# Kernel optimization log

Measured on AMD Instinct MI355X. Metric: run time of the kernel, lower is better.

The kernel has to match this reference:

```python
import jax, jax.numpy as jnp
import numpy as np

WINDOW_SYNC = 20   # min(20, T//2) with T=8192
WINDOW_SURGE = 10
BN_EPS = 1e-5      # BatchNorm1d eval-mode, running_mean=0, running_var=1


def _corr_matrix(x):
    # x: [w, A] observations x variables -> [A, A] Pearson correlation
    xc = x - x.mean(0)
    cov = xc.T @ xc
    d = jnp.sqrt(jnp.diag(cov))
    return cov / (d[:, None] * d[None, :])


def _offdiag_mean(C):
    A = C.shape[0]
    return (C.sum() - jnp.trace(C)) / (A * (A - 1))


def _rolling_offdiag_corr(returns, window):
    # mean off-diagonal correlation over each trailing window [i-window, i)
    T, A = returns.shape
    starts = jnp.arange(T - window)
    def one(s):
        w = jax.lax.dynamic_slice(returns, (s, 0), (window, A))
        return _offdiag_mean(_corr_matrix(w))
    return jax.vmap(one)(starts)


def setup_inputs() -> dict:
    key = jax.random.key(0)
    ks = jax.random.split(key, 10)
    T, A, H = 8192, 128, 128
    returns_sequence = jax.random.normal(ks[0], (T, A), dtype=jnp.float32) * 0.02
    positions = jax.random.normal(ks[1], (A,), dtype=jnp.float32)
    s1 = 1.0 / np.sqrt(2 * A)
    s2 = 1.0 / np.sqrt(H)
    s3 = 1.0 / np.sqrt(H // 2)
    return {
        "returns_sequence": returns_sequence,
        "positions": positions,
        "w1": jax.random.uniform(ks[2], (2 * A, H), jnp.float32, -s1, s1),
        "b1": jax.random.uniform(ks[3], (H,), jnp.float32, -s1, s1),
        "gamma": jnp.ones((H,), jnp.float32),
        "beta": jnp.zeros((H,), jnp.float32),
        "w2": jax.random.uniform(ks[4], (H, H // 2), jnp.float32, -s2, s2),
        "b2": jax.random.uniform(ks[5], (H // 2,), jnp.float32, -s2, s2),
        "w3": jax.random.uniform(ks[6], (H // 2, 3), jnp.float32, -s3, s3),
        "b3": jax.random.uniform(ks[7], (3,), jnp.float32, -s3, s3),
    }


def reference(returns_sequence, positions, w1, b1, gamma, beta, w2, b2, w3, b3):
    returns = returns_sequence
    T, A = returns.shape

    # ---- herding index ----
    cs_std = jnp.std(returns, axis=1, ddof=1)                 # [T]
    herding_trend = -jnp.diff(cs_std).mean()
    avg_dispersion = cs_std.mean()
    herding_index = jnp.clip(herding_trend / (avg_dispersion + 1e-6) + 0.5, 0.0, 1.0)

    # ---- synchronization ----
    corr = _corr_matrix(returns)                              # [A, A]
    avg_correlation = _offdiag_mean(corr)
    rolling = _rolling_offdiag_corr(returns, WINDOW_SYNC)     # [T-20]
    phase_locking = (rolling > 0.7).astype(jnp.float32).mean()
    eigvals = jnp.linalg.eigvalsh(corr)
    sync_indicator = eigvals.max() / A
    sync_risk = jnp.minimum(1.0, sync_indicator * avg_correlation)

    # ---- diversity loss ----
    return_diversity = 1.0 - jnp.abs(corr).mean()             # includes diagonal (as in torch)
    pa = jnp.abs(positions)
    position_diversity = 1.0 - (pa / pa.sum()).max()
    diversity_loss = 1.0 - jnp.sqrt(return_diversity * position_diversity)

    # ---- correlation surge ----
    rolling10 = _rolling_offdiag_corr(returns, WINDOW_SURGE)  # [T-10]
    recent = rolling10[-5:].mean()
    historical = rolling10[:-5].mean()
    surge_raw = jnp.clip((recent - historical) / historical, 0.0, 1.0)
    correlation_surge = jnp.where(historical > 0, surge_raw, 0.0)

    # ---- phase coupling (pairwise sign concordance) ----
    signs = jnp.sign(returns)                                 # [T, A]
    classes = jnp.array([-1.0, 0.0, 1.0], dtype=returns.dtype)
    I = (signs[None, :, :] == classes[:, None, None]).astype(returns.dtype)  # [3, T, A]
    M = jnp.einsum('cta,ctb->ab', I, I) / T                   # eq-fraction matrix [A, A]
    avg_concordance = _offdiag_mean(M)
    phase_coupling = jnp.clip((avg_concordance - 0.5) * 2.0, 0.0, 1.0)

    # ---- herding detector MLP (BatchNorm1d in eval mode) ----
    feats = jnp.concatenate([returns[-1], positions])         # [2A]
    h = jax.nn.relu(feats @ w1 + b1)
    h = gamma * (h / jnp.sqrt(1.0 + BN_EPS)) + beta
    h = jax.nn.relu(h @ w2 + b2)
    logits = h @ w3 + b3
    herding_severity = jax.nn.softmax(logits)[2]

    collective_risk = (herding_index + sync_risk + diversity_loss) / 3.0

    return jnp.stack([herding_index, herding_severity, sync_risk, phase_locking,
                      diversity_loss, correlation_surge, phase_coupling, collective_risk])
```

## Files before the change

kernel.cpp:

```cpp
#include <hip/hip_runtime.h>
#include <math.h>

#define TN 8192
#define AN 128
#define NW20 (TN - 20)
#define NW10 (TN - 10)

#define NB_GRAM 128
#define NB_ROW  512
#define NB_R20  511
#define NB_R10  512
#define NB_WORK (NB_GRAM + NB_ROW + NB_R20 + NB_R10)

#define WS_STD0 0
#define WS_STDL 1
#define WS_SPEC 8
#define WS_BLK  200
#define WS_DEND 4096

template <int W>
__device__ __forceinline__ void roll_strip4(const float* __restrict__ x,
                                            int s0, int nwin, int lane,
                                            double& accA, double& accB) {
  constexpr int NR = W + 3;
  float a0[NR], a1[NR];
#pragma unroll
  for (int t = 0; t < NR; ++t) {
    int r = s0 + t; r = (r < TN) ? r : (TN - 1);
    float2 v = *(const float2*)(x + (size_t)r * AN + 2 * lane);
    a0[t] = v.x; a1[t] = v.y;
  }
#pragma unroll
  for (int w4 = 0; w4 < 4; ++w4) {
    int s = s0 + w4;
    if (s < nwin) {
      float sf0 = 0.f, sf1 = 0.f;
#pragma unroll
      for (int t = 0; t < W; ++t) { sf0 += a0[w4 + t]; sf1 += a1[w4 + t]; }
      float mu0 = sf0 / W, mu1 = sf1 / W;
      float v0 = 0.f, v1 = 0.f;
#pragma unroll
      for (int t = 0; t < W; ++t) {
        float d0 = a0[w4 + t] - mu0, d1 = a1[w4 + t] - mu1;
        v0 += d0 * d0; v1 += d1 * d1;
      }
      float i0 = 1.0f / sqrtf(v0), i1 = 1.0f / sqrtf(v1);
      float q[W];
#pragma unroll
      for (int t = 0; t < W; ++t)
        q[t] = (a0[w4 + t] - mu0) * i0 + (a1[w4 + t] - mu1) * i1;
      int n = W;
#pragma unroll
      for (int o = 1; o <= 32; o <<= 1) {
#pragma unroll
        for (int k = 0; k < n; ++k) q[k] += __shfl_xor(q[k], o);
        if (n > 1) {
          int nh = n >> 1;
          bool hi = (lane & o) != 0;
#pragma unroll
          for (int k = 0; k < nh; ++k) q[k] = hi ? q[2 * k + 1] : q[2 * k];
          if (n & 1) { q[nh] = q[2 * nh]; n = nh + 1; } else { n = nh; }
        }
      }
      float alpha = (W == 20) ? ((lane & 16) ? 0.125f : 0.5f)
                              : ((lane & 8) ? 0.0625f : 0.25f);
      float r = q[0] * q[0] * alpha;
#pragma unroll
      for (int o = 32; o; o >>= 1) r += __shfl_xor(r, o);
      if (lane == 0) {
        double off = ((double)r - (double)AN) / ((double)AN * (AN - 1));
        if (W == 20) {
          accA += (off > 0.7) ? 1.0 : 0.0;
        } else {
          accA += off;
          if (s >= TN - W - 5) accB += off;
        }
      }
    }
  }
}

__global__ void __launch_bounds__(256) k_main(const float* __restrict__ x,
                                              double* __restrict__ wsd,
                                              float* __restrict__ pc,
                                              float* __restrict__ pdg,
                                              float* __restrict__ pg) {
  __shared__ union {
    float stage[8][AN];
    double tacc[4][2];
  } sm;
  const int b = blockIdx.x;
  const int tid = threadIdx.x;
  const int lane = tid & 63;
  const int w = tid >> 6;

  if (b < NB_GRAM) {
    int i0 = (tid >> 4) * 8;
    int j0 = (tid & 15) * 8;
    int lrow = tid >> 5;
    int lcol = (tid & 31) * 4;
    const float* xs = x + (size_t)b * 64 * AN;
    float acc[8][8];
#pragma unroll
    for (int a = 0; a < 8; ++a)
#pragma unroll
      for (int c = 0; c < 8; ++c) acc[a][c] = 0.f;
    float4 v = *(const float4*)(xs + lrow * AN + lcol);
    for (int it = 0; it < 8; ++it) {
      __syncthreads();
      *(float4*)(&sm.stage[lrow][lcol]) = v;
      __syncthreads();
      if (it + 1 < 8)
        v = *(const float4*)(xs + ((it + 1) * 8 + lrow) * AN + lcol);
#pragma unroll
      for (int r = 0; r < 8; ++r) {
        float aa[8], bb[8];
        *(float4*)(aa) = *(const float4*)(&sm.stage[r][i0]);
        *(float4*)(aa + 4) = *(const float4*)(&sm.stage[r][i0 + 4]);
        *(float4*)(bb) = *(const float4*)(&sm.stage[r][j0]);
        *(float4*)(bb + 4) = *(const float4*)(&sm.stage[r][j0 + 4]);
#pragma unroll
        for (int ai = 0; ai < 8; ++ai)
#pragma unroll
          for (int bj = 0; bj < 8; ++bj)
            acc[ai][bj] = fmaf(aa[ai], bb[bj], acc[ai][bj]);
      }
    }
    float* dst = pg + (size_t)b * (AN * AN);
#pragma unroll
    for (int ai = 0; ai < 8; ++ai)
#pragma unroll
      for (int bj = 0; bj < 8; bj += 4)
        *(float4*)(dst + (i0 + ai) * AN + j0 + bj) =
            make_float4(acc[ai][bj], acc[ai][bj + 1], acc[ai][bj + 2],
                        acc[ai][bj + 3]);
    if ((tid >> 4) == (tid & 15)) {
#pragma unroll
      for (int k = 0; k < 8; ++k) pdg[b * AN + i0 + k] = acc[k][k];
    }
    if (tid < AN) {
      float cs = 0.f;
      for (int r = 0; r < 64; ++r) cs += xs[r * AN + tid];
      pc[b * AN + tid] = cs;
    }
    return;
  }

  if (b < NB_GRAM + NB_ROW) {
    int rb = b - NB_GRAM;
    double sstd = 0.0, sconc = 0.0;
    for (int rr = 0; rr < 4; ++rr) {
      int t = rb * 16 + w * 4 + rr;
      float2 xv = *(const float2*)(x + (size_t)t * AN + 2 * lane);
      float x0 = xv.x, x1 = xv.y;
      float s = x0 + x1;
#pragma unroll
      for (int o = 32; o; o >>= 1) s += __shfl_xor(s, o);
      float mean = s * (1.0f / AN);
      float d0 = x0 - mean, d1 = x1 - mean;
      float q = d0 * d0 + d1 * d1;
#pragma unroll
      for (int o = 32; o; o >>= 1) q += __shfl_xor(q, o);
      float sd = sqrtf(q / (float)(AN - 1));
      int pk = (int)(x0 < 0.f) + (int)(x1 < 0.f)
             + (((int)(x0 == 0.f) + (int)(x1 == 0.f)) << 10)
             + (((int)(x0 > 0.f) + (int)(x1 > 0.f)) << 20);
#pragma unroll
      for (int o = 32; o; o >>= 1) pk += __shfl_xor(pk, o);
      if (lane == 0) {
        int nn = pk & 1023, nz = (pk >> 10) & 1023, np = (pk >> 20) & 1023;
        sconc += (double)nn * nn + (double)nz * nz + (double)np * np;
        sstd += (double)sd;
        if (t == 0) wsd[WS_STD0] = (double)sd;
        if (t == TN - 1) wsd[WS_STDL] = (double)sd;
      }
    }
    if (lane == 0) { sm.tacc[w][0] = sstd; sm.tacc[w][1] = sconc; }
    __syncthreads();
    if (tid == 0) {
      wsd[WS_BLK + (size_t)b * 2 + 0] =
          sm.tacc[0][0] + sm.tacc[1][0] + sm.tacc[2][0] + sm.tacc[3][0];
      wsd[WS_BLK + (size_t)b * 2 + 1] =
          sm.tacc[0][1] + sm.tacc[1][1] + sm.tacc[2][1] + sm.tacc[3][1];
    }
    return;
  }

  if (b < NB_GRAM + NB_ROW + NB_R20) {
    int s0 = (b - (NB_GRAM + NB_ROW)) * 16 + w * 4;
    double cnt = 0.0, dummy = 0.0;
    roll_strip4<20>(x, s0, NW20, lane, cnt, dummy);
    if (lane == 0) { sm.tacc[w][0] = cnt; }
    __syncthreads();
    if (tid == 0)
      wsd[WS_BLK + (size_t)b * 2 + 0] =
          sm.tacc[0][0] + sm.tacc[1][0] + sm.tacc[2][0] + sm.tacc[3][0];
    return;
  }

  {
    int s0 = (b - (NB_GRAM + NB_ROW + NB_R20)) * 16 + w * 4;
    double s10 = 0.0, s10l5 = 0.0;
    roll_strip4<10>(x, s0, NW10, lane, s10, s10l5);
    if (lane == 0) { sm.tacc[w][0] = s10; sm.tacc[w][1] = s10l5; }
    __syncthreads();
    if (tid == 0) {
      wsd[WS_BLK + (size_t)b * 2 + 0] =
          sm.tacc[0][0] + sm.tacc[1][0] + sm.tacc[2][0] + sm.tacc[3][0];
      wsd[WS_BLK + (size_t)b * 2 + 1] =
          sm.tacc[0][1] + sm.tacc[1][1] + sm.tacc[2][1] + sm.tacc[3][1];
    }
  }
}

__global__ void __launch_bounds__(256) k_fold(const float* __restrict__ pc,
                                              const float* __restrict__ pdg,
                                              const float* __restrict__ pg,
                                              double* __restrict__ wsd,
                                              float* __restrict__ corr) {
  __shared__ double r0[256], r1[256], r2[256], r3[256], r4[256];
  int b = blockIdx.x;
  int t = threadIdx.x;
  if (b < 64) {
    __shared__ double muS[AN], dS[AN];
    if (t < AN) {
      double cs = 0.0, dg = 0.0;
      for (int s = 0; s < NB_GRAM; ++s) {
        cs += (double)pc[s * AN + t];
        dg += (double)pdg[s * AN + t];
      }
      double mu = cs / (double)TN;
      muS[t] = mu;
      dS[t] = sqrt(dg - (double)TN * mu * mu);
    }
    __syncthreads();
    int e = b * 256 + t;
    int i = e >> 7, j = e & (AN - 1);
    double cv = 0.0;
    for (int s = 0; s < NB_GRAM; ++s) cv += (double)pg[(size_t)s * (AN * AN) + e];
    cv -= (double)TN * muS[i] * muS[j];
    double c = cv / (dS[i] * dS[j]);
    corr[e] = (float)c;
    r0[t] = c;
    r1[t] = fabs(c);
    r2[t] = (i == j) ? c : 0.0;
    __syncthreads();
    for (int sft = 128; sft; sft >>= 1) {
      if (t < sft) { r0[t] += r0[t + sft]; r1[t] += r1[t + sft]; r2[t] += r2[t + sft]; }
      __syncthreads();
    }
    if (t == 0) {
      wsd[WS_SPEC + b * 3 + 0] = r0[0];
      wsd[WS_SPEC + b * 3 + 1] = r1[0];
      wsd[WS_SPEC + b * 3 + 2] = r2[0];
    }
  } else {
    double a = 0.0, bc = 0.0, cnt = 0.0, s10 = 0.0, s10l5 = 0.0;
    for (int k = NB_GRAM + t; k < NB_WORK; k += 256) {
      const double* p = wsd + WS_BLK + (size_t)k * 2;
      if (k < NB_GRAM + NB_ROW) { a += p[0]; bc += p[1]; }
      else if (k < NB_GRAM + NB_ROW + NB_R20) cnt += p[0];
      else { s10 += p[0]; s10l5 += p[1]; }
    }
    r0[t] = a; r1[t] = bc; r2[t] = cnt; r3[t] = s10; r4[t] = s10l5;
    __syncthreads();
    for (int sft = 128; sft; sft >>= 1) {
      if (t < sft) {
        r0[t] += r0[t + sft]; r1[t] += r1[t + sft]; r2[t] += r2[t + sft];
        r3[t] += r3[t + sft]; r4[t] += r4[t + sft];
      }
      __syncthreads();
    }
    if (t == 0) {
      wsd[2] = r0[0];
      wsd[3] = r1[0];
      wsd[4] = r2[0];
      wsd[5] = r3[0];
      wsd[6] = r4[0];
    }
  }
}

__global__ void __launch_bounds__(256) k_spec_tail(
    const float* __restrict__ x, const float* __restrict__ pos,
    const float* __restrict__ w1, const float* __restrict__ b1,
    const float* __restrict__ gamma, const float* __restrict__ beta,
    const float* __restrict__ w2, const float* __restrict__ b2,
    const float* __restrict__ w3, const float* __restrict__ b3,
    const double* __restrict__ wsd, const float* __restrict__ corr,
    float* __restrict__ out) {
  __shared__ float vv[AN], prt[256], un[AN], red[4];
  __shared__ double spec[3];
  __shared__ float f[2 * AN], h1[AN], h2[64], lg[3];
  int t = threadIdx.x;
  int lane = t & 63;
  int w = t >> 6;
  if (t < 64) {
    double s0 = wsd[WS_SPEC + t * 3 + 0];
    double s1 = wsd[WS_SPEC + t * 3 + 1];
    double s2 = wsd[WS_SPEC + t * 3 + 2];
#pragma unroll
    for (int o = 32; o; o >>= 1) {
      s0 += __shfl_xor(s0, o);
      s1 += __shfl_xor(s1, o);
      s2 += __shfl_xor(s2, o);
    }
    if (t == 0) { spec[0] = s0; spec[1] = s1; spec[2] = s2; }
  }
  f[t] = (t < AN) ? x[(size_t)(TN - 1) * AN + t] : pos[t - AN];
  if (t < AN) vv[t] = 1.0f;
  __syncthreads();
  int ri = t & (AN - 1), hh = t >> 7;
  const float4* rp = (const float4*)(corr + ri * AN + hh * 64);
  float lam = 0.0f;
  for (int it = 0; it < 12; ++it) {
    const float4* vp = (const float4*)(&vv[hh * 64]);
    float acc = 0.f;
#pragma unroll
    for (int k = 0; k < 16; ++k) {
      float4 a = rp[k], bv = vp[k];
      acc += a.x * bv.x + a.y * bv.y + a.z * bv.z + a.w * bv.w;
    }
    prt[t] = acc;
    __syncthreads();
    if (t < AN) {
      float u = prt[t] + prt[t + 128];
      un[t] = u;
      float sq = u * u;
#pragma unroll
      for (int o = 32; o; o >>= 1) sq += __shfl_xor(sq, o);
      if (lane == 0) red[w] = sq;
    }
    __syncthreads();
    lam = sqrtf(red[0] + red[1]);
    if (t < AN) vv[t] = un[t] / lam;
    __syncthreads();
  }
  {
    int n = t & 127, h = t >> 7;
    float acc = 0.f;
    const float* wcol = w1 + h * 128 * AN + n;
    const float* fv = f + h * 128;
    for (int k = 0; k < 128; ++k) acc = fmaf(fv[k], wcol[k * AN], acc);
    prt[t] = acc;
  }
  __syncthreads();
  if (t < AN) {
    float acc = b1[t] + prt[t] + prt[t + 128];
    acc = fmaxf(acc, 0.0f);
    h1[t] = gamma[t] * (acc / sqrtf(1.0f + 1e-5f)) + beta[t];
  }
  __syncthreads();
  if (t < 64) {
    float acc = b2[t];
    for (int k = 0; k < AN; ++k) acc = fmaf(h1[k], w2[k * 64 + t], acc);
    h2[t] = fmaxf(acc, 0.0f);
  }
  __syncthreads();
  if (t < 3) {
    float acc = b3[t];
    for (int k = 0; k < 64; ++k) acc = fmaf(h2[k], w3[k * 3 + t], acc);
    lg[t] = acc;
  }
  __syncthreads();
  if (t != 0) return;
  float m = fmaxf(lg[0], fmaxf(lg[1], lg[2]));
  float e0 = expf(lg[0] - m), e1 = expf(lg[1] - m), e2 = expf(lg[2] - m);
  double sev = (double)(e2 / (e0 + e1 + e2));
  double sumstd = wsd[2], conc = wsd[3], cnt20 = wsd[4];
  double sum10 = wsd[5], sum10l5 = wsd[6];
  double avg_disp = sumstd / (double)TN;
  double trend = -(wsd[WS_STDL] - wsd[WS_STD0]) / (double)(TN - 1);
  double hi = trend / (avg_disp + 1e-6) + 0.5;
  hi = fmin(1.0, fmax(0.0, hi));
  double avg_corr = (spec[0] - spec[2]) / ((double)AN * (AN - 1));
  double sync_ind = (double)lam / (double)AN;
  double sync_risk = fmin(1.0, sync_ind * avg_corr);
  double pl = cnt20 / (double)(TN - 20);
  double rd = 1.0 - spec[1] / ((double)AN * AN);
  double pasum = 0.0, pamax = 0.0;
  for (int k = 0; k < AN; ++k) {
    double pa = fabs((double)pos[k]);
    pasum += pa;
    if (pa > pamax) pamax = pa;
  }
  double pd = 1.0 - pamax / pasum;
  double dl = 1.0 - sqrt(rd * pd);
  double recent = sum10l5 / 5.0;
  double hist = (sum10 - sum10l5) / (double)(TN - 10 - 5);
  double sraw = (recent - hist) / hist;
  sraw = fmin(1.0, fmax(0.0, sraw));
  double surge = (hist > 0.0) ? sraw : 0.0;
  double ac = (conc / (double)TN - (double)AN) / ((double)AN * (AN - 1));
  double pcup = fmin(1.0, fmax(0.0, (ac - 0.5) * 2.0));
  double cr = (hi + sync_risk + dl) / 3.0;
  out[0] = (float)hi;
  out[1] = (float)sev;
  out[2] = (float)sync_risk;
  out[3] = (float)pl;
  out[4] = (float)dl;
  out[5] = (float)surge;
  out[6] = (float)pcup;
  out[7] = (float)cr;
}

extern "C" void kernel_launch(void* const* d_in, const int* in_sizes, int n_in,
                              void* d_out, int out_size, void* d_ws, size_t ws_size,
                              hipStream_t stream) {
  const float* x     = (const float*)d_in[0];
  const float* pos   = (const float*)d_in[1];
  const float* w1    = (const float*)d_in[2];
  const float* b1    = (const float*)d_in[3];
  const float* gamma = (const float*)d_in[4];
  const float* beta  = (const float*)d_in[5];
  const float* w2    = (const float*)d_in[6];
  const float* b2    = (const float*)d_in[7];
  const float* w3    = (const float*)d_in[8];
  const float* b3    = (const float*)d_in[9];
  float* out = (float*)d_out;
  double* wsd = (double*)d_ws;
  float* corr = (float*)(wsd + WS_DEND);
  float* pc   = corr + AN * AN;
  float* pdg  = pc + NB_GRAM * AN;
  float* pg   = pdg + NB_GRAM * AN;

  k_main<<<NB_WORK, 256, 0, stream>>>(x, wsd, pc, pdg, pg);
  k_fold<<<65, 256, 0, stream>>>(pc, pdg, pg, wsd, corr);
  k_spec_tail<<<1, 256, 0, stream>>>(x, pos, w1, b1, gamma, beta, w2, b2,
                                     w3, b3, wsd, corr, out);
}
```

Baseline: 127.1 us.

## Merge fold and spectral tail kernels using an atomic completion flag

After: 183.5 us. 1.44x slower.

```diff
diff --git a/kernel.cpp b/kernel.cpp
--- a/kernel.cpp
+++ b/kernel.cpp
@@ -14,6 +14,7 @@
 
 #define WS_STD0 0
 #define WS_STDL 1
+#define WS_FLAG 7
 #define WS_SPEC 8
 #define WS_BLK  200
 #define WS_DEND 4096
@@ -94,6 +95,8 @@
   const int lane = tid & 63;
   const int w = tid >> 6;
 
+  if (b == 0 && tid == 0) *(int*)(wsd + WS_FLAG) = 0;
+
   if (b < NB_GRAM) {
     int i0 = (tid >> 4) * 8;
     int j0 = (tid & 15) * 8;
@@ -213,14 +216,22 @@
   }
 }
 
-__global__ void __launch_bounds__(256) k_fold(const float* __restrict__ pc,
-                                              const float* __restrict__ pdg,
-                                              const float* __restrict__ pg,
-                                              double* __restrict__ wsd,
-                                              float* __restrict__ corr) {
+__global__ void __launch_bounds__(256) k_tail(
+    const float* __restrict__ x, const float* __restrict__ pos,
+    const float* __restrict__ w1, const float* __restrict__ b1,
+    const float* __restrict__ gamma, const float* __restrict__ beta,
+    const float* __restrict__ w2, const float* __restrict__ b2,
+    const float* __restrict__ w3, const float* __restrict__ b3,
+    const float* __restrict__ pc, const float* __restrict__ pdg,
+    const float* __restrict__ pg, double* __restrict__ wsd,
+    float* __restrict__ corr, float* __restrict__ out) {
   __shared__ double r0[256], r1[256], r2[256], r3[256], r4[256];
   int b = blockIdx.x;
   int t = threadIdx.x;
+  int lane = t & 63;
+  int w = t >> 6;
+  int* flg = (int*)(wsd + WS_FLAG);
+
   if (b < 64) {
     __shared__ double muS[AN], dS[AN];
     if (t < AN) {
@@ -254,7 +265,17 @@
       wsd[WS_SPEC + b * 3 + 1] = r1[0];
       wsd[WS_SPEC + b * 3 + 2] = r2[0];
     }
-  } else {
+    __syncthreads();
+    if (t == 0)
+      __hip_atomic_fetch_add(flg, 1, __ATOMIC_RELEASE, __HIP_MEMORY_SCOPE_AGENT);
+    return;
+  }
+
+  __shared__ float f[2 * AN], prt[256], h1[AN], h2[64], lg[3];
+  __shared__ float vv[AN], un[AN], red[4];
+  __shared__ double spec[3], scv[8], pr2[4];
+
+  {
     double a = 0.0, bc = 0.0, cnt = 0.0, s10 = 0.0, s10l5 = 0.0;
     for (int k = NB_GRAM + t; k < NB_WORK; k += 256) {
       const double* p = wsd + WS_BLK + (size_t)k * 2;
@@ -272,70 +293,16 @@
       __syncthreads();
     }
     if (t == 0) {
-      wsd[2] = r0[0];
-      wsd[3] = r1[0];
-      wsd[4] = r2[0];
-      wsd[5] = r3[0];
-      wsd[6] = r4[0];
-    }
-  }
-}
-
-__global__ void __launch_bounds__(256) k_spec_tail(
-    const float* __restrict__ x, const float* __restrict__ pos,
-    const float* __restrict__ w1, const float* __restrict__ b1,
-    const float* __restrict__ gamma, const float* __restrict__ beta,
-    const float* __restrict__ w2, const float* __restrict__ b2,
-    const float* __restrict__ w3, const float* __restrict__ b3,
-    const double* __restrict__ wsd, const float* __restrict__ corr,
-    float* __restrict__ out) {
-  __shared__ float vv[AN], prt[256], un[AN], red[4];
-  __shared__ double spec[3];
-  __shared__ float f[2 * AN], h1[AN], h2[64], lg[3];
-  int t = threadIdx.x;
-  int lane = t & 63;
-  int w = t >> 6;
-  if (t < 64) {
-    double s0 = wsd[WS_SPEC + t * 3 + 0];
-    double s1 = wsd[WS_SPEC + t * 3 + 1];
-    double s2 = wsd[WS_SPEC + t * 3 + 2];
-#pragma unroll
-    for (int o = 32; o; o >>= 1) {
-      s0 += __shfl_xor(s0, o);
-      s1 += __shfl_xor(s1, o);
-      s2 += __shfl_xor(s2, o);
-    }
-    if (t == 0) { spec[0] = s0; spec[1] = s1; spec[2] = s2; }
-  }
+      scv[0] = r0[0];
+      scv[1] = r1[0];
+      scv[2] = r2[0];
+      scv[3] = r3[0];
+      scv[4] = r4[0];
+    }
+  }
+
   f[t] = (t < AN) ? x[(size_t)(TN - 1) * AN + t] : pos[t - AN];
-  if (t < AN) vv[t] = 1.0f;
-  __syncthreads();
-  int ri = t & (AN - 1), hh = t >> 7;
-  const float4* rp = (const float4*)(corr + ri * AN + hh * 64);
-  float lam = 0.0f;
-  for (int it = 0; it < 12; ++it) {
-    const float4* vp = (const float4*)(&vv[hh * 64]);
-    float acc = 0.f;
-#pragma unroll
-    for (int k = 0; k < 16; ++k) {
-      float4 a = rp[k], bv = vp[k];
-      acc += a.x * bv.x + a.y * bv.y + a.z * bv.z + a.w * bv.w;
-    }
-    prt[t] = acc;
-    __syncthreads();
-    if (t < AN) {
-      float u = prt[t] + prt[t + 128];
-      un[t] = u;
-      float sq = u * u;
-#pragma unroll
-      for (int o = 32; o; o >>= 1) sq += __shfl_xor(sq, o);
-      if (lane == 0) red[w] = sq;
-    }
-    __syncthreads();
-    lam = sqrtf(red[0] + red[1]);
-    if (t < AN) vv[t] = un[t] / lam;
-    __syncthreads();
-  }
+  __syncthreads();
   {
     int n = t & 127, h = t >> 7;
     float acc = 0.f;
@@ -362,13 +329,76 @@
     for (int k = 0; k < 64; ++k) acc = fmaf(h2[k], w3[k * 3 + t], acc);
     lg[t] = acc;
   }
-  __syncthreads();
+
+  if (t < AN) {
+    double pa = fabs((double)pos[t]);
+    double ps = pa, pm = pa;
+#pragma unroll
+    for (int o = 32; o; o >>= 1) {
+      ps += __shfl_xor(ps, o);
+      pm = fmax(pm, __shfl_xor(pm, o));
+    }
+    if (lane == 0) { pr2[w] = ps; pr2[2 + w] = pm; }
+  }
+  __syncthreads();
+  if (t == 0) {
+    float m = fmaxf(lg[0], fmaxf(lg[1], lg[2]));
+    float e0 = expf(lg[0] - m), e1 = expf(lg[1] - m), e2 = expf(lg[2] - m);
+    scv[5] = (double)(e2 / (e0 + e1 + e2));
+    scv[6] = pr2[0] + pr2[1];
+    scv[7] = fmax(pr2[2], pr2[3]);
+  }
+
+  if (t == 0) {
+    while (__hip_atomic_load(flg, __ATOMIC_RELAXED, __HIP_MEMORY_SCOPE_AGENT) < 64)
+      __builtin_amdgcn_s_sleep(2);
+    (void)__hip_atomic_load(flg, __ATOMIC_ACQUIRE, __HIP_MEMORY_SCOPE_AGENT);
+  }
+  __syncthreads();
+
+  if (t < 64) {
+    double s0 = wsd[WS_SPEC + t * 3 + 0];
+    double s1 = wsd[WS_SPEC + t * 3 + 1];
+    double s2 = wsd[WS_SPEC + t * 3 + 2];
+#pragma unroll
+    for (int o = 32; o; o >>= 1) {
+      s0 += __shfl_xor(s0, o);
+      s1 += __shfl_xor(s1, o);
+      s2 += __shfl_xor(s2, o);
+    }
+    if (t == 0) { spec[0] = s0; spec[1] = s1; spec[2] = s2; }
+  }
+  if (t < AN) vv[t] = 1.0f;
+  __syncthreads();
+
+  int c = t & (AN - 1), hh = t >> 7;
+  const float* cp = corr + (size_t)hh * 64 * AN + c;
+  float lam = 0.0f;
+  for (int it = 0; it < 12; ++it) {
+    float acc = 0.f;
+#pragma unroll
+    for (int k = 0; k < 64; ++k)
+      acc = fmaf(cp[(size_t)k * AN], vv[hh * 64 + k], acc);
+    prt[t] = acc;
+    __syncthreads();
+    if (t < AN) {
+      float u = prt[t] + prt[t + 128];
+      un[t] = u;
+      float sq = u * u;
+#pragma unroll
+      for (int o = 32; o; o >>= 1) sq += __shfl_xor(sq, o);
+      if (lane == 0) red[w] = sq;
+    }
+    __syncthreads();
+    lam = sqrtf(red[0] + red[1]);
+    if (t < AN) vv[t] = un[t] / lam;
+    __syncthreads();
+  }
+
   if (t != 0) return;
-  float m = fmaxf(lg[0], fmaxf(lg[1], lg[2]));
-  float e0 = expf(lg[0] - m), e1 = expf(lg[1] - m), e2 = expf(lg[2] - m);
-  double sev = (double)(e2 / (e0 + e1 + e2));
-  double sumstd = wsd[2], conc = wsd[3], cnt20 = wsd[4];
-  double sum10 = wsd[5], sum10l5 = wsd[6];
+  double sev = scv[5];
+  double sumstd = scv[0], conc = scv[1], cnt20 = scv[2];
+  double sum10 = scv[3], sum10l5 = scv[4];
   double avg_disp = sumstd / (double)TN;
   double trend = -(wsd[WS_STDL] - wsd[WS_STD0]) / (double)(TN - 1);
   double hi = trend / (avg_disp + 1e-6) + 0.5;
@@ -378,13 +408,7 @@
   double sync_risk = fmin(1.0, sync_ind * avg_corr);
   double pl = cnt20 / (double)(TN - 20);
   double rd = 1.0 - spec[1] / ((double)AN * AN);
-  double pasum = 0.0, pamax = 0.0;
-  for (int k = 0; k < AN; ++k) {
-    double pa = fabs((double)pos[k]);
-    pasum += pa;
-    if (pa > pamax) pamax = pa;
-  }
-  double pd = 1.0 - pamax / pasum;
+  double pd = 1.0 - scv[7] / scv[6];
   double dl = 1.0 - sqrt(rd * pd);
   double recent = sum10l5 / 5.0;
   double hist = (sum10 - sum10l5) / (double)(TN - 10 - 5);
@@ -425,7 +449,6 @@
   float* pg   = pdg + NB_GRAM * AN;
 
   k_main<<<NB_WORK, 256, 0, stream>>>(x, wsd, pc, pdg, pg);
-  k_fold<<<65, 256, 0, stream>>>(pc, pdg, pg, wsd, corr);
-  k_spec_tail<<<1, 256, 0, stream>>>(x, pos, w1, b1, gamma, beta, w2, b2,
-                                     w3, b3, wsd, corr, out);
+  k_tail<<<65, 256, 0, stream>>>(x, pos, w1, b1, gamma, beta, w2, b2,
+                                 w3, b3, pc, pdg, pg, wsd, corr, out);
 }
```
